# Kernel tuning notes

Measured on AMD Instinct MI355X. Metric: run time of the kernel, lower is better.

## Reference

```python
import jax, jax.numpy as jnp
import numpy as np

EPS = 1e-5

def layernorm(x, w, b):
    m = jnp.mean(x, axis=-1, keepdims=True)
    v = jnp.var(x, axis=-1, keepdims=True)
    return (x - m) * jax.lax.rsqrt(v + EPS) * w + b

def setup_inputs() -> dict:
    key = jax.random.key(0)
    ks = jax.random.split(key, 20)
    B, N, D, H, C = 4, 2048, 512, 8, 3
    HID = int(D * 4.0 * (2.0 / 3.0))  # SwiGLU hidden = 1365
    g = lambda k, shape, s: (jax.random.normal(k, shape, jnp.float32) * s)
    return {
        "x": g(ks[0], (B, N, D), 1.0),
        "coords": jax.random.uniform(ks[1], (B, N, C), jnp.float32),
        "ln1_w": jnp.ones((D,), jnp.float32),
        "ln1_b": jnp.zeros((D,), jnp.float32),
        "ln2_w": jnp.ones((D,), jnp.float32),
        "ln2_b": jnp.zeros((D,), jnp.float32),
        "Wqkv": g(ks[2], (D, 3 * D), D ** -0.5),
        "bqkv": jnp.zeros((3 * D,), jnp.float32),
        "Wo": g(ks[3], (D, D), D ** -0.5),
        "bo": jnp.zeros((D,), jnp.float32),
        "Wc": g(ks[4], (C, H), 0.1),
        "bc": jnp.zeros((H,), jnp.float32),
        "W1": g(ks[5], (D, HID), D ** -0.5),
        "b1": jnp.zeros((HID,), jnp.float32),
        "W2": g(ks[6], (D, HID), D ** -0.5),
        "b2": jnp.zeros((HID,), jnp.float32),
        "W3": g(ks[7], (HID, D), HID ** -0.5),
        "b3": jnp.zeros((D,), jnp.float32),
    }

def reference(x, coords, ln1_w, ln1_b, ln2_w, ln2_b, Wqkv, bqkv, Wo, bo,
              Wc, bc, W1, b1, W2, b2, W3, b3):
    B, N, D = x.shape
    H = bc.shape[0]
    dh = D // H
    # --- coord-aware patch attention (pre-norm) ---
    h = layernorm(x, ln1_w, ln1_b)
    qkv = h @ Wqkv + bqkv                                # [B,N,3D]
    q, k, v = jnp.split(qkv, 3, axis=-1)
    to_heads = lambda t: t.reshape(B, N, H, dh).transpose(0, 2, 1, 3)  # [B,H,N,dh]
    q, k, v = to_heads(q), to_heads(k), to_heads(v)
    scores = jnp.einsum("bhnd,bhmd->bhnm", q, k) / np.sqrt(dh)
    rel = coords[:, :, None, :] - coords[:, None, :, :]  # [B,N,N,C]
    bias = jnp.einsum("bnmc,ch->bhnm", rel, Wc) + bc[None, :, None, None]
    attn = jax.nn.softmax(scores + bias, axis=-1)
    o = jnp.einsum("bhnm,bhmd->bhnd", attn, v)
    o = o.transpose(0, 2, 1, 3).reshape(B, N, D)
    x = x + (o @ Wo + bo)                                # residual 1
    # --- SwiGLU FFN (pre-norm) ---
    h2 = layernorm(x, ln2_w, ln2_b)
    ff = jax.nn.silu(h2 @ W1 + b1) * (h2 @ W2 + b2)
    x = x + (ff @ W3 + b3)                               # residual 2
    return x
```

## Files before the change

### kernel.cpp

```cpp
#include <hip/hip_runtime.h>
#include <hip/hip_bf16.h>
#include <math.h>

#define B_   4
#define N_   2048
#define D_   512
#define H_   8
#define DH_  64
#define C_   3
#define HID_ 1365
#define HIDP 1408
#define ROWS_ (B_*N_)
#define TD_  (3*D_)

typedef __attribute__((ext_vector_type(8))) short short8;
typedef __attribute__((ext_vector_type(4))) float floatx4;
typedef __attribute__((ext_vector_type(2))) unsigned uint2v;

#define MFMA16(a,b,c) __builtin_amdgcn_mfma_f32_16x16x32_bf16(a,b,c,0,0,0)

typedef __attribute__((address_space(3))) unsigned lds_u32;
typedef __attribute__((address_space(1))) unsigned glb_u32;

__device__ __forceinline__ short sh(float v){
  union { __hip_bfloat16 b; short s; } u;
  u.b = __float2bfloat16(v);
  return u.s;
}

__device__ __forceinline__ unsigned pk2(float a, float b){
  union { short s[2]; unsigned u; } z;
  z.s[0] = sh(a); z.s[1] = sh(b);
  return z.u;
}

__device__ __forceinline__ int swz(int col, int row){
  return (col & ~63) | (col & 7) | ((((col >> 3) & 7) ^ (row & 7)) << 3);
}

template<int ROWS, int PITCH>
__device__ __forceinline__ void stageG(short* __restrict__ lds,
    const short* __restrict__ g, int ldg, int t){
  const int LPR = PITCH/8;
  const int RPI = 64/LPR;
  const int PW  = (ROWS/RPI)/4;
  int lane = t & 63, w = t >> 6;
  #pragma unroll
  for (int i = 0; i < PW; ++i){
    int r0  = (w*PW + i)*RPI;
    int row = r0 + lane/LPR;
    const short* ga = g + (size_t)row*ldg + (lane % LPR)*8;
    short* la = lds + r0*PITCH;
    __builtin_amdgcn_global_load_lds((const glb_u32*)ga, (lds_u32*)la, 16, 0, 0);
  }
}

__device__ __forceinline__ short8 fragS(const short* __restrict__ lds, int pitch,
    int mbase, int lane, int kk){
  int row  = mbase + (lane & 15);
  int seg  = (kk >> 3) + (lane >> 4);
  int phys = seg ^ (row & 7);
  return *(const short8*)(lds + row*pitch + phys*8);
}

__global__ __launch_bounds__(256) void convT_all(
    const float* __restrict__ Wqkv, const float* __restrict__ Wo,
    const float* __restrict__ W1, const float* __restrict__ W2,
    const float* __restrict__ W3,
    short* __restrict__ Wtqkv, short* __restrict__ Wto,
    short* __restrict__ Wt1, short* __restrict__ Wt2, short* __restrict__ Wt3,
    const float* __restrict__ coords, const float* __restrict__ Wc,
    float* __restrict__ tv,
    const float* __restrict__ x, const float* __restrict__ ln1_w,
    const float* __restrict__ ln1_b, short* __restrict__ h){
  int id = blockIdx.x;
  int t = threadIdx.x;
  if (id >= 3392){
    int row = id - 3392;
    size_t base = (size_t)row * D_;
    float v0 = x[base + t];
    float v1 = x[base + t + 256];
    float s  = v0 + v1;
    float s2 = v0*v0 + v1*v1;
    #pragma unroll
    for (int off = 32; off >= 1; off >>= 1){
      s  += __shfl_xor(s,  off, 64);
      s2 += __shfl_xor(s2, off, 64);
    }
    __shared__ float red[8];
    int lane = t & 63, wv = t >> 6;
    if (lane == 0){ red[wv] = s; red[4+wv] = s2; }
    __syncthreads();
    float sum  = red[0]+red[1]+red[2]+red[3];
    float sum2 = red[4]+red[5]+red[6]+red[7];
    float mean = sum * (1.0f/D_);
    float var  = sum2 * (1.0f/D_) - mean*mean;
    float inv  = rsqrtf(fmaxf(var, 0.f) + 1e-5f);
    h[base + swz(t,     row)] = sh((v0-mean)*inv*ln1_w[t]     + ln1_b[t]);
    h[base + swz(t+256, row)] = sh((v1-mean)*inv*ln1_w[t+256] + ln1_b[t+256]);
    return;
  }
  if (id >= 3136){
    int idx = (id - 3136)*256 + t;
    int n = idx & (N_-1);
    int hh = (idx >> 11) & (H_-1);
    int b = idx >> 14;
    float s = 0.f;
    #pragma unroll
    for (int cc = 0; cc < C_; ++cc)
      s += coords[((size_t)(b*N_+n))*C_ + cc] * Wc[cc*H_ + hh];
    tv[idx] = s;
    return;
  }
  __shared__ float tile[32][33];
  const float* in; short* out; int K, NN, Kp, nx;
  if (id < 768)      { in=Wqkv; out=Wtqkv; K=512;  NN=1536; Kp=512;  nx=48; }
  else if (id < 1024){ in=Wo;   out=Wto;   K=512;  NN=512;  Kp=512;  nx=16; id-=768; }
  else if (id < 1728){ in=W1;   out=Wt1;   K=512;  NN=HID_; Kp=512;  nx=44; id-=1024; }
  else if (id < 2432){ in=W2;   out=Wt2;   K=512;  NN=HID_; Kp=512;  nx=44; id-=1728; }
  else               { in=W3;   out=Wt3;   K=HID_; NN=512;  Kp=HIDP; nx=16; id-=2432; }
  int nt0 = (id % nx)*32, kt0 = (id / nx)*32;
  int r = t >> 5, cc = t & 31;
  #pragma unroll
  for (int i=0;i<4;++i){
    int k = kt0 + i*8 + r, n = nt0 + cc;
    tile[i*8+r][cc] = (k<K && n<NN) ? in[(size_t)k*NN + n] : 0.f;
  }
  __syncthreads();
  #pragma unroll
  for (int i=0;i<4;++i){
    int n = nt0 + i*8 + r, k = kt0 + cc;
    out[(size_t)n*Kp + swz(k, n)] = sh(tile[cc][i*8+r]);
  }
}

__global__ __launch_bounds__(256) void ln_kernel(const float* __restrict__ x,
        const float* __restrict__ w, const float* __restrict__ b,
        short* __restrict__ out){
  int row = blockIdx.x;
  size_t base = (size_t)row * D_;
  int t = threadIdx.x;
  float v0 = x[base + t];
  float v1 = x[base + t + 256];
  float s  = v0 + v1;
  float s2 = v0*v0 + v1*v1;
  #pragma unroll
  for (int off = 32; off >= 1; off >>= 1){
    s  += __shfl_xor(s,  off, 64);
    s2 += __shfl_xor(s2, off, 64);
  }
  __shared__ float red[8];
  int lane = t & 63, wv = t >> 6;
  if (lane == 0){ red[wv] = s; red[4+wv] = s2; }
  __syncthreads();
  float sum  = red[0]+red[1]+red[2]+red[3];
  float sum2 = red[4]+red[5]+red[6]+red[7];
  float mean = sum * (1.0f/D_);
  float var  = sum2 * (1.0f/D_) - mean*mean;
  float inv  = rsqrtf(fmaxf(var, 0.f) + 1e-5f);
  out[base + swz(t,     row)] = sh((v0-mean)*inv*w[t]     + b[t]);
  out[base + swz(t+256, row)] = sh((v1-mean)*inv*w[t+256] + b[t+256]);
}

__global__ __launch_bounds__(256) void qkv_gemm(
    const short* __restrict__ A, const short* __restrict__ Bt,
    const float* __restrict__ bias,
    short* __restrict__ qb, short* __restrict__ kb, short* __restrict__ vbt){
  __shared__ short As[128*64];
  __shared__ short Bs[128*64];
  int t = threadIdx.x;
  int lane = t & 63, w = t >> 6;
  int wr = (w >> 1) * 64, wc = (w & 1) * 64;
  int col0 = blockIdx.x * 128, row0 = blockIdx.y * 128;
  floatx4 acc[4][4];
  #pragma unroll
  for (int mt=0;mt<4;++mt)
    #pragma unroll
    for (int nt=0;nt<4;++nt) acc[mt][nt] = (floatx4){0.f,0.f,0.f,0.f};
  for (int k0 = 0; k0 < D_; k0 += 64){
    __syncthreads();
    stageG<128,64>(As, A  + (size_t)row0*D_ + k0, D_, t);
    stageG<128,64>(Bs, Bt + (size_t)col0*D_ + k0, D_, t);
    __syncthreads();
    #pragma unroll
    for (int kk = 0; kk < 64; kk += 32){
      short8 af[4], bf[4];
      #pragma unroll
      for (int mt=0;mt<4;++mt) af[mt] = fragS(As, 64, wr+mt*16, lane, kk);
      #pragma unroll
      for (int nt=0;nt<4;++nt) bf[nt] = fragS(Bs, 64, wc+nt*16, lane, kk);
      #pragma unroll
      for (int mt=0;mt<4;++mt)
        #pragma unroll
        for (int nt=0;nt<4;++nt)
          acc[mt][nt] = MFMA16(af[mt], bf[nt], acc[mt][nt]);
    }
  }
  int quad = lane >> 4, c = lane & 15;
  #pragma unroll
  for (int mt=0;mt<4;++mt){
    #pragma unroll
    for (int nt=0;nt<4;++nt){
      #pragma unroll
      for (int r=0;r<4;++r){
        int row = row0 + wr + mt*16 + quad*4 + r;
        int col = col0 + wc + nt*16 + c;
        float v = acc[mt][nt][r] + bias[col];
        int bidx = row >> 11, n = row & (N_-1);
        int which = col >> 9, d = col & (D_-1), hh = d >> 6, hd = d & 63;
        short sv = sh(v);
        if (which == 0)
          qb[(((size_t)(bidx*H_ + hh))*N_ + n)*DH_ + swz(hd, n)] = sv;
        else if (which == 1)
          kb[(((size_t)(bidx*H_ + hh))*N_ + n)*DH_ + swz(hd, n)] = sv;
        else
          vbt[(((size_t)(bidx*H_ + hh))*DH_ + hd)*N_ + swz(n, hd)] = sv;
      }
    }
  }
}

__global__ __launch_bounds__(256) void gemm64(
    const short* __restrict__ A, int lda,
    const short* __restrict__ Bt, int Ktot,
    const float* __restrict__ bias,
    const float* __restrict__ resid, float* __restrict__ outF){
  __shared__ short As[128*64];
  __shared__ short Bs[64*64];
  int t = threadIdx.x, lane = t & 63, w = t >> 6;
  int wr = w * 32;
  int col0 = blockIdx.x * 64, row0 = blockIdx.y * 128;
  floatx4 acc[2][4];
  #pragma unroll
  for (int mt=0;mt<2;++mt)
    #pragma unroll
    for (int nt=0;nt<4;++nt) acc[mt][nt] = (floatx4){0.f,0.f,0.f,0.f};
  for (int k0 = 0; k0 < Ktot; k0 += 64){
    __syncthreads();
    stageG<128,64>(As, A  + (size_t)row0*lda + k0, lda, t);
    stageG<64,64> (Bs, Bt + (size_t)col0*Ktot + k0, Ktot, t);
    __syncthreads();
    #pragma unroll
    for (int kk = 0; kk < 64; kk += 32){
      short8 af[2], bf[4];
      #pragma unroll
      for (int mt=0;mt<2;++mt) af[mt] = fragS(As, 64, wr+mt*16, lane, kk);
      #pragma unroll
      for (int nt=0;nt<4;++nt) bf[nt] = fragS(Bs, 64, nt*16, lane, kk);
      #pragma unroll
      for (int mt=0;mt<2;++mt)
        #pragma unroll
        for (int nt=0;nt<4;++nt)
          acc[mt][nt] = MFMA16(af[mt], bf[nt], acc[mt][nt]);
    }
  }
  int quad = lane >> 4, c = lane & 15;
  #pragma unroll
  for (int mt=0;mt<2;++mt){
    #pragma unroll
    for (int nt=0;nt<4;++nt){
      #pragma unroll
      for (int r=0;r<4;++r){
        int row = row0 + wr + mt*16 + quad*4 + r;
        int col = col0 + nt*16 + c;
        size_t idx = (size_t)row*D_ + col;
        outF[idx] = acc[mt][nt][r] + bias[col] + resid[idx];
      }
    }
  }
}

__global__ __launch_bounds__(256) void gate_gemm(
    const short* __restrict__ A,
    const short* __restrict__ Bt1, const short* __restrict__ Bt2,
    const float* __restrict__ b1, const float* __restrict__ b2,
    short* __restrict__ ff){
  __shared__ short As[128*64];
  __shared__ short B1s[64*64];
  __shared__ short B2s[64*64];
  int t = threadIdx.x, lane = t & 63, w = t >> 6;
  int wr = (w >> 1) * 64, wc = (w & 1) * 32;
  int col0 = blockIdx.x * 64, row0 = blockIdx.y * 128;
  floatx4 a1[4][2], a2[4][2];
  #pragma unroll
  for (int mt=0;mt<4;++mt)
    #pragma unroll
    for (int nt=0;nt<2;++nt){
      a1[mt][nt] = (floatx4){0.f,0.f,0.f,0.f};
      a2[mt][nt] = (floatx4){0.f,0.f,0.f,0.f};
    }
  for (int k0 = 0; k0 < D_; k0 += 64){
    __syncthreads();
    stageG<128,64>(As, A + (size_t)row0*D_ + k0, D_, t);
    stageG<64,64>(B1s, Bt1 + (size_t)col0*D_ + k0, D_, t);
    stageG<64,64>(B2s, Bt2 + (size_t)col0*D_ + k0, D_, t);
    __syncthreads();
    #pragma unroll
    for (int kk = 0; kk < 64; kk += 32){
      short8 af[4], f1[2], f2[2];
      #pragma unroll
      for (int mt=0;mt<4;++mt) af[mt] = fragS(As, 64, wr+mt*16, lane, kk);
      #pragma unroll
      for (int nt=0;nt<2;++nt){
        f1[nt] = fragS(B1s, 64, wc+nt*16, lane, kk);
        f2[nt] = fragS(B2s, 64, wc+nt*16, lane, kk);
      }
      #pragma unroll
      for (int mt=0;mt<4;++mt)
        #pragma unroll
        for (int nt=0;nt<2;++nt){
          a1[mt][nt] = MFMA16(af[mt], f1[nt], a1[mt][nt]);
          a2[mt][nt] = MFMA16(af[mt], f2[nt], a2[mt][nt]);
        }
    }
  }
  int quad = lane >> 4, c = lane & 15;
  #pragma unroll
  for (int mt=0;mt<4;++mt){
    #pragma unroll
    for (int nt=0;nt<2;++nt){
      #pragma unroll
      for (int r=0;r<4;++r){
        int row = row0 + wr + mt*16 + quad*4 + r;
        int col = col0 + wc + nt*16 + c;
        float g1 = a1[mt][nt][r] + (col < HID_ ? b1[col] : 0.f);
        float g2 = a2[mt][nt][r] + (col < HID_ ? b2[col] : 0.f);
        float sig = 1.f / (1.f + __expf(-g1));
        ff[(size_t)row*HIDP + swz(col, row)] = sh(g1*sig*g2);
      }
    }
  }
}

#define EXP2SC 0.18033688011112042f
__global__ __launch_bounds__(256) void attn_mfma(
    const short* __restrict__ qb, const short* __restrict__ kbuf,
    const short* __restrict__ vbt, const float* __restrict__ tv,
    short* __restrict__ o){
  __shared__ short Ks2[2][128*64];
  __shared__ short Vt2[2][64*128];
  __shared__ __align__(16) float tsAll[2048];
  int qt = blockIdx.x, h = blockIdx.y, b = blockIdx.z;
  int bh = b*H_ + h;
  int t = threadIdx.x, lane = t & 63, w = t >> 6;
  int quad = lane >> 4, c = lane & 15;
  const short* Kbase = kbuf + (size_t)bh*N_*DH_;
  const short* Vbase = vbt  + (size_t)bh*DH_*N_;

  #pragma unroll
  for (int i = 0; i < 8; ++i)
    tsAll[i*256 + t] = tv[(size_t)bh*N_ + i*256 + t] * 1.44269504f;
  stageG<128,64>(Ks2[1], qb + ((size_t)bh*N_ + qt*128)*DH_, DH_, t);
  stageG<128,64>(Ks2[0], Kbase, DH_, t);
  stageG<64,128>(Vt2[0], Vbase, N_, t);
  __syncthreads();
  short8 qf[2][2];
  #pragma unroll
  for (int mt=0;mt<2;++mt)
    #pragma unroll
    for (int kh=0;kh<2;++kh)
      qf[mt][kh] = fragS(Ks2[1], 64, w*32 + mt*16, lane, kh*32);
  floatx4 O[2][4];
  float l_i[2] = {0.f, 0.f};
  #pragma unroll
  for (int mt=0;mt<2;++mt)
    #pragma unroll
    for (int nt=0;nt<4;++nt) O[mt][nt] = (floatx4){0.f,0.f,0.f,0.f};
  __syncthreads();

  for (int kt = 0; kt < N_/128; ++kt){
    int cur = kt & 1;
    if (kt + 1 < N_/128){
      stageG<128,64>(Ks2[cur^1], Kbase + (size_t)(kt+1)*128*DH_, DH_, t);
      stageG<64,128>(Vt2[cur^1], Vbase + (kt+1)*128, N_, t);
    }
    const short* Kc  = Ks2[cur];
    const short* Vc  = Vt2[cur];
    const float* tsc = tsAll + kt*128;
    #pragma unroll
    for (int kb4 = 0; kb4 < 4; ++kb4){
      floatx4 St[2][2];
      #pragma unroll
      for (int i=0;i<2;++i){
        St[i][0] = (floatx4){0.f,0.f,0.f,0.f};
        St[i][1] = (floatx4){0.f,0.f,0.f,0.f};
      }
      #pragma unroll
      for (int kh=0;kh<2;++kh){
        short8 kf0 = fragS(Kc, 64, kb4*32,      lane, kh*32);
        short8 kf1 = fragS(Kc, 64, kb4*32 + 16, lane, kh*32);
        #pragma unroll
        for (int mt=0;mt<2;++mt){
          St[0][mt] = MFMA16(kf0, qf[mt][kh], St[0][mt]);
          St[1][mt] = MFMA16(kf1, qf[mt][kh], St[1][mt]);
        }
      }
      floatx4 t0 = *(const floatx4*)&tsc[kb4*32 + quad*4];
      floatx4 t1 = *(const floatx4*)&tsc[kb4*32 + 16 + quad*4];
      short8 pbf[2];
      #pragma unroll
      for (int mt=0;mt<2;++mt){
        float p0[4], p1[4];
        #pragma unroll
        for (int r=0;r<4;++r){
          p0[r] = __builtin_amdgcn_exp2f(fmaf(St[0][mt][r], EXP2SC, -t0[r]));
          p1[r] = __builtin_amdgcn_exp2f(fmaf(St[1][mt][r], EXP2SC, -t1[r]));
        }
        l_i[mt] += (p0[0]+p0[1]) + (p0[2]+p0[3]) + (p1[0]+p1[1]) + (p1[2]+p1[3]);
        unsigned X0 = pk2(p0[0], p0[1]), X1 = pk2(p0[2], p0[3]);
        unsigned Y0 = pk2(p1[0], p1[1]), Y1 = pk2(p1[2], p1[3]);
        auto u0 = __builtin_amdgcn_permlane32_swap(X0, Y0, false, false);
        auto v0 = __builtin_amdgcn_permlane16_swap(u0[0], u0[1], false, false);
        auto u1 = __builtin_amdgcn_permlane32_swap(X1, Y1, false, false);
        auto v1 = __builtin_amdgcn_permlane16_swap(u1[0], u1[1], false, false);
        union { short8 s; unsigned uu[4]; } pb;
        pb.uu[0] = v0[0]; pb.uu[1] = v1[0]; pb.uu[2] = v0[1]; pb.uu[3] = v1[1];
        pbf[mt] = pb.s;
      }
      #pragma unroll
      for (int nt=0;nt<4;++nt){
        short8 vf = fragS(Vc, 128, nt*16, lane, kb4*32);
        #pragma unroll
        for (int mt=0;mt<2;++mt)
          O[mt][nt] = MFMA16(vf, pbf[mt], O[mt][nt]);
      }
    }
    __syncthreads();
  }
  #pragma unroll
  for (int mt=0;mt<2;++mt){
    float l = l_i[mt];
    l += __shfl_xor(l, 16, 64);
    l += __shfl_xor(l, 32, 64);
    float invl = 1.f / l;
    int qrow = qt*128 + w*32 + mt*16 + c;
    size_t rb = ((size_t)b*N_ + qrow)*(size_t)D_;
    #pragma unroll
    for (int nt=0;nt<4;++nt){
      int d0 = h*DH_ + nt*16 + quad*4;
      uint2v pv;
      pv.x = pk2(O[mt][nt][0]*invl, O[mt][nt][1]*invl);
      pv.y = pk2(O[mt][nt][2]*invl, O[mt][nt][3]*invl);
      *(uint2v*)(o + rb + swz(d0, qrow)) = pv;
    }
  }
}

extern "C" void kernel_launch(void* const* d_in, const int* in_sizes, int n_in,
                              void* d_out, int out_size, void* d_ws, size_t ws_size,
                              hipStream_t stream){
  const float* x      = (const float*)d_in[0];
  const float* coords = (const float*)d_in[1];
  const float* ln1_w  = (const float*)d_in[2];
  const float* ln1_b  = (const float*)d_in[3];
  const float* ln2_w  = (const float*)d_in[4];
  const float* ln2_b  = (const float*)d_in[5];
  const float* Wqkv   = (const float*)d_in[6];
  const float* bqkv   = (const float*)d_in[7];
  const float* Wo     = (const float*)d_in[8];
  const float* bo     = (const float*)d_in[9];
  const float* Wc     = (const float*)d_in[10];
  const float* W1     = (const float*)d_in[12];
  const float* b1     = (const float*)d_in[13];
  const float* W2     = (const float*)d_in[14];
  const float* b2     = (const float*)d_in[15];
  const float* W3     = (const float*)d_in[16];
  const float* b3     = (const float*)d_in[17];

  char* ws = (char*)d_ws;
  short* Wtqkv = (short*)(ws);
  short* Wto   = (short*)(ws + 1572864);
  short* Wt1   = (short*)(ws + 2097152);
  short* Wt2   = (short*)(ws + 3538944);
  short* Wt3   = (short*)(ws + 4980736);
  float* tv    = (float*)(ws + 6422528);
  short* h     = (short*)(ws + 6684672);
  short* qb    = (short*)(ws + 15073280);
  short* kb    = (short*)(ws + 23461888);
  short* vbt   = (short*)(ws + 31850496);
  short* o     = h;
  short* h2    = h;
  short* ff    = qb;
  float* x1    = (float*)d_out;

  convT_all<<<dim3(11584), dim3(256), 0, stream>>>(Wqkv, Wo, W1, W2, W3,
      Wtqkv, Wto, Wt1, Wt2, Wt3, coords, Wc, tv, x, ln1_w, ln1_b, h);
  qkv_gemm<<<dim3(12,64), dim3(256), 0, stream>>>(h, Wtqkv, bqkv, qb, kb, vbt);
  attn_mfma<<<dim3(16,8,4), dim3(256), 0, stream>>>(qb, kb, vbt, tv, o);
  gemm64<<<dim3(8,64), dim3(256), 0, stream>>>(o, 512, Wto, 512, bo, x, x1);
  ln_kernel<<<dim3(ROWS_), dim3(256), 0, stream>>>(x1, ln2_w, ln2_b, h2);
  gate_gemm<<<dim3(22,64), dim3(256), 0, stream>>>(h2, Wt1, Wt2, b1, b2, ff);
  gemm64<<<dim3(8,64), dim3(256), 0, stream>>>(ff, HIDP, Wt3, HIDP, b3, x1, x1);
}
```

Baseline: 310.8 us.

## Split attention keys across two wave groups, enlarge GEMM tiles to 128x128

The attention kernel now runs 512 threads, with two groups of four waves each handling half of every key tile. The two partial O and l results are merged through LDS at the end, and the log2e scaling of the coord bias moves into the precompute kernel. The output-projection, W3 and gate GEMMs move from 64-wide to 128-wide column tiles with 4x4 MFMA tiles per wave. This gives more data reuse per block but fewer blocks and more registers and LDS per block. The attention split is meant to add parallelism and hide latency within a block, at the cost of an extra reduction and a larger register budget under launch_bounds(512,4).

Result: slower. 360.1 us (+15.9%).

```diff
diff --git a/kernel.cpp b/kernel.cpp
--- a/kernel.cpp
+++ b/kernel.cpp
@@ -38,12 +38,12 @@
   return (col & ~63) | (col & 7) | ((((col >> 3) & 7) ^ (row & 7)) << 3);
 }
 
-template<int ROWS, int PITCH>
+template<int ROWS, int PITCH, int WAVES = 4>
 __device__ __forceinline__ void stageG(short* __restrict__ lds,
     const short* __restrict__ g, int ldg, int t){
   const int LPR = PITCH/8;
   const int RPI = 64/LPR;
-  const int PW  = (ROWS/RPI)/4;
+  const int PW  = (ROWS/RPI)/WAVES;
   int lane = t & 63, w = t >> 6;
   #pragma unroll
   for (int i = 0; i < PW; ++i){
@@ -109,7 +109,7 @@
     #pragma unroll
     for (int cc = 0; cc < C_; ++cc)
       s += coords[((size_t)(b*N_+n))*C_ + cc] * Wc[cc*H_ + hh];
-    tv[idx] = s;
+    tv[idx] = s * 1.44269504f;
     return;
   }
   __shared__ float tile[32][33];
@@ -220,35 +220,35 @@
   }
 }
 
-__global__ __launch_bounds__(256) void gemm64(
+__global__ __launch_bounds__(256) void gemm128(
     const short* __restrict__ A, int lda,
     const short* __restrict__ Bt, int Ktot,
     const float* __restrict__ bias,
     const float* __restrict__ resid, float* __restrict__ outF){
   __shared__ short As[128*64];
-  __shared__ short Bs[64*64];
+  __shared__ short Bs[128*64];
   int t = threadIdx.x, lane = t & 63, w = t >> 6;
-  int wr = w * 32;
-  int col0 = blockIdx.x * 64, row0 = blockIdx.y * 128;
-  floatx4 acc[2][4];
-  #pragma unroll
-  for (int mt=0;mt<2;++mt)
+  int wr = (w >> 1) * 64, wc = (w & 1) * 64;
+  int col0 = blockIdx.x * 128, row0 = blockIdx.y * 128;
+  floatx4 acc[4][4];
+  #pragma unroll
+  for (int mt=0;mt<4;++mt)
     #pragma unroll
     for (int nt=0;nt<4;++nt) acc[mt][nt] = (floatx4){0.f,0.f,0.f,0.f};
   for (int k0 = 0; k0 < Ktot; k0 += 64){
     __syncthreads();
     stageG<128,64>(As, A  + (size_t)row0*lda + k0, lda, t);
-    stageG<64,64> (Bs, Bt + (size_t)col0*Ktot + k0, Ktot, t);
+    stageG<128,64>(Bs, Bt + (size_t)col0*Ktot + k0, Ktot, t);
     __syncthreads();
     #pragma unroll
     for (int kk = 0; kk < 64; kk += 32){
-      short8 af[2], bf[4];
-      #pragma unroll
-      for (int mt=0;mt<2;++mt) af[mt] = fragS(As, 64, wr+mt*16, lane, kk);
-      #pragma unroll
-      for (int nt=0;nt<4;++nt) bf[nt] = fragS(Bs, 64, nt*16, lane, kk);
-      #pragma unroll
-      for (int mt=0;mt<2;++mt)
+      short8 af[4], bf[4];
+      #pragma unroll
+      for (int mt=0;mt<4;++mt) af[mt] = fragS(As, 64, wr+mt*16, lane, kk);
+      #pragma unroll
+      for (int nt=0;nt<4;++nt) bf[nt] = fragS(Bs, 64, wc+nt*16, lane, kk);
+      #pragma unroll
+      for (int mt=0;mt<4;++mt)
         #pragma unroll
         for (int nt=0;nt<4;++nt)
           acc[mt][nt] = MFMA16(af[mt], bf[nt], acc[mt][nt]);
@@ -256,13 +256,13 @@
   }
   int quad = lane >> 4, c = lane & 15;
   #pragma unroll
-  for (int mt=0;mt<2;++mt){
+  for (int mt=0;mt<4;++mt){
     #pragma unroll
     for (int nt=0;nt<4;++nt){
       #pragma unroll
       for (int r=0;r<4;++r){
         int row = row0 + wr + mt*16 + quad*4 + r;
-        int col = col0 + nt*16 + c;
+        int col = col0 + wc + nt*16 + c;
         size_t idx = (size_t)row*D_ + col;
         outF[idx] = acc[mt][nt][r] + bias[col] + resid[idx];
       }
@@ -276,39 +276,39 @@
     const float* __restrict__ b1, const float* __restrict__ b2,
     short* __restrict__ ff){
   __shared__ short As[128*64];
-  __shared__ short B1s[64*64];
-  __shared__ short B2s[64*64];
+  __shared__ short B1s[128*64];
+  __shared__ short B2s[128*64];
   int t = threadIdx.x, lane = t & 63, w = t >> 6;
-  int wr = (w >> 1) * 64, wc = (w & 1) * 32;
-  int col0 = blockIdx.x * 64, row0 = blockIdx.y * 128;
-  floatx4 a1[4][2], a2[4][2];
+  int wr = (w >> 1) * 64, wc = (w & 1) * 64;
+  int col0 = blockIdx.x * 128, row0 = blockIdx.y * 128;
+  floatx4 a1[4][4], a2[4][4];
   #pragma unroll
   for (int mt=0;mt<4;++mt)
     #pragma unroll
-    for (int nt=0;nt<2;++nt){
+    for (int nt=0;nt<4;++nt){
       a1[mt][nt] = (floatx4){0.f,0.f,0.f,0.f};
       a2[mt][nt] = (floatx4){0.f,0.f,0.f,0.f};
     }
   for (int k0 = 0; k0 < D_; k0 += 64){
     __syncthreads();
     stageG<128,64>(As, A + (size_t)row0*D_ + k0, D_, t);
-    stageG<64,64>(B1s, Bt1 + (size_t)col0*D_ + k0, D_, t);
-    stageG<64,64>(B2s, Bt2 + (size_t)col0*D_ + k0, D_, t);
+    stageG<128,64>(B1s, Bt1 + (size_t)col0*D_ + k0, D_, t);
+    stageG<128,64>(B2s, Bt2 + (size_t)col0*D_ + k0, D_, t);
     __syncthreads();
     #pragma unroll
     for (int kk = 0; kk < 64; kk += 32){
-      short8 af[4], f1[2], f2[2];
+      short8 af[4], f1[4], f2[4];
       #pragma unroll
       for (int mt=0;mt<4;++mt) af[mt] = fragS(As, 64, wr+mt*16, lane, kk);
       #pragma unroll
-      for (int nt=0;nt<2;++nt){
+      for (int nt=0;nt<4;++nt){
         f1[nt] = fragS(B1s, 64, wc+nt*16, lane, kk);
         f2[nt] = fragS(B2s, 64, wc+nt*16, lane, kk);
       }
       #pragma unroll
       for (int mt=0;mt<4;++mt)
         #pragma unroll
-        for (int nt=0;nt<2;++nt){
+        for (int nt=0;nt<4;++nt){
           a1[mt][nt] = MFMA16(af[mt], f1[nt], a1[mt][nt]);
           a2[mt][nt] = MFMA16(af[mt], f2[nt], a2[mt][nt]);
         }
@@ -318,7 +318,7 @@
   #pragma unroll
   for (int mt=0;mt<4;++mt){
     #pragma unroll
-    for (int nt=0;nt<2;++nt){
+    for (int nt=0;nt<4;++nt){
       #pragma unroll
       for (int r=0;r<4;++r){
         int row = row0 + wr + mt*16 + quad*4 + r;
@@ -333,7 +333,7 @@
 }
 
 #define EXP2SC 0.18033688011112042f
-__global__ __launch_bounds__(256) void attn_mfma(
+__global__ __launch_bounds__(512,4) void attn_mfma(
     const short* __restrict__ qb, const short* __restrict__ kbuf,
     const short* __restrict__ vbt, const float* __restrict__ tv,
     short* __restrict__ o){
@@ -343,23 +343,22 @@
   int qt = blockIdx.x, h = blockIdx.y, b = blockIdx.z;
   int bh = b*H_ + h;
   int t = threadIdx.x, lane = t & 63, w = t >> 6;
+  int qg = w & 3, kg = w >> 2;
   int quad = lane >> 4, c = lane & 15;
   const short* Kbase = kbuf + (size_t)bh*N_*DH_;
   const short* Vbase = vbt  + (size_t)bh*DH_*N_;
 
-  #pragma unroll
-  for (int i = 0; i < 8; ++i)
-    tsAll[i*256 + t] = tv[(size_t)bh*N_ + i*256 + t] * 1.44269504f;
-  stageG<128,64>(Ks2[1], qb + ((size_t)bh*N_ + qt*128)*DH_, DH_, t);
-  stageG<128,64>(Ks2[0], Kbase, DH_, t);
-  stageG<64,128>(Vt2[0], Vbase, N_, t);
+  *(floatx4*)&tsAll[t*4] = *(const floatx4*)&tv[(size_t)bh*N_ + t*4];
+  stageG<128,64,8>(Ks2[1], qb + ((size_t)bh*N_ + qt*128)*DH_, DH_, t);
+  stageG<128,64,8>(Ks2[0], Kbase, DH_, t);
+  stageG<64,128,8>(Vt2[0], Vbase, N_, t);
   __syncthreads();
   short8 qf[2][2];
   #pragma unroll
   for (int mt=0;mt<2;++mt)
     #pragma unroll
     for (int kh=0;kh<2;++kh)
-      qf[mt][kh] = fragS(Ks2[1], 64, w*32 + mt*16, lane, kh*32);
+      qf[mt][kh] = fragS(Ks2[1], 64, qg*32 + mt*16, lane, kh*32);
   floatx4 O[2][4];
   float l_i[2] = {0.f, 0.f};
   #pragma unroll
@@ -371,14 +370,15 @@
   for (int kt = 0; kt < N_/128; ++kt){
     int cur = kt & 1;
     if (kt + 1 < N_/128){
-      stageG<128,64>(Ks2[cur^1], Kbase + (size_t)(kt+1)*128*DH_, DH_, t);
-      stageG<64,128>(Vt2[cur^1], Vbase + (kt+1)*128, N_, t);
+      stageG<128,64,8>(Ks2[cur^1], Kbase + (size_t)(kt+1)*128*DH_, DH_, t);
+      stageG<64,128,8>(Vt2[cur^1], Vbase + (kt+1)*128, N_, t);
     }
     const short* Kc  = Ks2[cur];
     const short* Vc  = Vt2[cur];
     const float* tsc = tsAll + kt*128;
     #pragma unroll
-    for (int kb4 = 0; kb4 < 4; ++kb4){
+    for (int kb = 0; kb < 2; ++kb){
+      int kb4 = kg*2 + kb;
       floatx4 St[2][2];
       #pragma unroll
       for (int i=0;i<2;++i){
@@ -427,21 +427,42 @@
     }
     __syncthreads();
   }
-  #pragma unroll
-  for (int mt=0;mt<2;++mt){
-    float l = l_i[mt];
-    l += __shfl_xor(l, 16, 64);
-    l += __shfl_xor(l, 32, 64);
-    float invl = 1.f / l;
-    int qrow = qt*128 + w*32 + mt*16 + c;
-    size_t rb = ((size_t)b*N_ + qrow)*(size_t)D_;
-    #pragma unroll
-    for (int nt=0;nt<4;++nt){
-      int d0 = h*DH_ + nt*16 + quad*4;
-      uint2v pv;
-      pv.x = pk2(O[mt][nt][0]*invl, O[mt][nt][1]*invl);
-      pv.y = pk2(O[mt][nt][2]*invl, O[mt][nt][3]*invl);
-      *(uint2v*)(o + rb + swz(d0, qrow)) = pv;
+  float* Om = (float*)Vt2;
+  float* Lm = (float*)Ks2;
+  if (kg == 1){
+    #pragma unroll
+    for (int mt=0;mt<2;++mt){
+      #pragma unroll
+      for (int nt=0;nt<4;++nt)
+        *(floatx4*)&Om[(((qg*2+mt)*4+nt)*64 + lane)*4] = O[mt][nt];
+      Lm[(qg*2+mt)*64 + lane] = l_i[mt];
+    }
+  }
+  __syncthreads();
+  if (kg == 0){
+    #pragma unroll
+    for (int mt=0;mt<2;++mt){
+      l_i[mt] += Lm[(qg*2+mt)*64 + lane];
+      #pragma unroll
+      for (int nt=0;nt<4;++nt)
+        O[mt][nt] += *(const floatx4*)&Om[(((qg*2+mt)*4+nt)*64 + lane)*4];
+    }
+    #pragma unroll
+    for (int mt=0;mt<2;++mt){
+      float l = l_i[mt];
+      l += __shfl_xor(l, 16, 64);
+      l += __shfl_xor(l, 32, 64);
+      float invl = 1.f / l;
+      int qrow = qt*128 + qg*32 + mt*16 + c;
+      size_t rb = ((size_t)b*N_ + qrow)*(size_t)D_;
+      #pragma unroll
+      for (int nt=0;nt<4;++nt){
+        int d0 = h*DH_ + nt*16 + quad*4;
+        uint2v pv;
+        pv.x = pk2(O[mt][nt][0]*invl, O[mt][nt][1]*invl);
+        pv.y = pk2(O[mt][nt][2]*invl, O[mt][nt][3]*invl);
+        *(uint2v*)(o + rb + swz(d0, qrow)) = pv;
+      }
     }
   }
 }
@@ -486,9 +507,9 @@
   convT_all<<<dim3(11584), dim3(256), 0, stream>>>(Wqkv, Wo, W1, W2, W3,
       Wtqkv, Wto, Wt1, Wt2, Wt3, coords, Wc, tv, x, ln1_w, ln1_b, h);
   qkv_gemm<<<dim3(12,64), dim3(256), 0, stream>>>(h, Wtqkv, bqkv, qb, kb, vbt);
-  attn_mfma<<<dim3(16,8,4), dim3(256), 0, stream>>>(qb, kb, vbt, tv, o);
-  gemm64<<<dim3(8,64), dim3(256), 0, stream>>>(o, 512, Wto, 512, bo, x, x1);
+  attn_mfma<<<dim3(16,8,4), dim3(512), 0, stream>>>(qb, kb, vbt, tv, o);
+  gemm128<<<dim3(4,64), dim3(256), 0, stream>>>(o, 512, Wto, 512, bo, x, x1);
   ln_kernel<<<dim3(ROWS_), dim3(256), 0, stream>>>(x1, ln2_w, ln2_b, h2);
-  gate_gemm<<<dim3(22,64), dim3(256), 0, stream>>>(h2, Wt1, Wt2, b1, b2, ff);
-  gemm64<<<dim3(8,64), dim3(256), 0, stream>>>(ff, HIDP, Wt3, HIDP, b3, x1, x1);
-}
+  gate_gemm<<<dim3(11,64), dim3(256), 0, stream>>>(h2, Wt1, Wt2, b1, b2, ff);
+  gemm128<<<dim3(4,64), dim3(256), 0, stream>>>(ff, HIDP, Wt3, HIDP, b3, x1, x1);
+}
```
